# Optimization experiments

Hardware: AMD Instinct MI355X
Metric: run time of the kernel (lower is better)

The kernel has to match this reference:

```python
import jax, jax.numpy as jnp
import numpy as np

B, S, E = 4, 2048, 1024
H, HD, R = 16, 64, 32  # heads, head_dim, rank


def setup_inputs() -> dict:
    key = jax.random.key(0)
    ks = jax.random.split(key, 9)
    sc = 0.02
    return {
        "hidden_states": jax.random.normal(ks[0], (B, S, E), jnp.float32),
        "q_weight": jax.random.normal(ks[1], (E, E), jnp.float32) * sc,
        "q_bias": jax.random.normal(ks[2], (E,), jnp.float32) * sc,
        "k_weight": jax.random.normal(ks[3], (E, E), jnp.float32) * sc,
        "k_bias": jax.random.normal(ks[4], (E,), jnp.float32) * sc,
        "low_rank_value_weight": jax.random.normal(ks[5], (E, H * R), jnp.float32) * sc,
        "low_rank_value_bias": jax.random.normal(ks[6], (H * R,), jnp.float32) * sc,
        "low_rank_output_weight": jax.random.normal(ks[7], (H * R, E), jnp.float32) * sc,
        "output_bias": jax.random.normal(ks[8], (E,), jnp.float32) * sc,
    }


def reference(hidden_states, q_weight, q_bias, k_weight, k_bias,
              low_rank_value_weight, low_rank_value_bias,
              low_rank_output_weight, output_bias):
    b, s, _ = hidden_states.shape
    q = hidden_states @ q_weight + q_bias                       # [B,S,E]
    k = hidden_states @ k_weight + k_bias                       # [B,S,E]
    v = hidden_states @ low_rank_value_weight + low_rank_value_bias  # [B,S,H*R]
    q = q.reshape(b, s, H, HD).transpose(0, 2, 1, 3)            # [B,H,S,HD]
    k = k.reshape(b, s, H, HD).transpose(0, 2, 1, 3)
    v = v.reshape(b, s, H, R).transpose(0, 2, 1, 3)             # [B,H,S,R]
    scores = jnp.einsum('bhqd,bhkd->bhqk', q, k) / jnp.sqrt(jnp.float32(HD))
    causal = jnp.tril(jnp.ones((s, s), dtype=bool))
    scores = jnp.where(causal, scores, jnp.finfo(scores.dtype).min)
    probs = jax.nn.softmax(scores, axis=-1)                     # [B,H,S,S]
    attn = jnp.einsum('bhqk,bhkr->bhqr', probs, v)              # [B,H,S,R]
    attn = attn.transpose(0, 2, 1, 3).reshape(b, s, H * R)      # [B,S,H*R]
    out = attn @ low_rank_output_weight + output_bias           # [B,S,E]
    return out
```

## Files before the change

kernel.cpp:

```cpp
#include <hip/hip_runtime.h>

typedef _Float16 f16;
typedef __attribute__((ext_vector_type(4))) float f4;
typedef __attribute__((ext_vector_type(4))) _Float16 h4;
typedef __attribute__((ext_vector_type(8))) _Float16 h8;
typedef __attribute__((ext_vector_type(4))) float f32x4;
typedef __attribute__((ext_vector_type(4))) unsigned int u4;

extern "C" __device__ __attribute__((const)) float __ocml_native_exp2_f32(float);
#define EXP2F __ocml_native_exp2_f32
#define L2E 1.4426950408889634f

#define SWZ(row, colByte) \
  (((row) << 7) + ((colByte) ^ (((((row) ^ ((row) >> 3))) & 7) << 4)))

__global__ __launch_bounds__(256) void prep(
    const float* __restrict__ hs, f16* __restrict__ hsf,
    const float* __restrict__ qw, const float* __restrict__ kw,
    const float* __restrict__ vw, const float* __restrict__ ow,
    f16* __restrict__ wqkv, f16* __restrict__ owt) {
  const int t = threadIdx.x;
  if (blockIdx.x < 2048) {
    const int n4 = 8192 * 1024 / 4;
    for (int i = blockIdx.x * 256 + t; i < n4; i += 2048 * 256) {
      const f4 v = ((const f4*)hs)[i];
      h4 h;
      h.x = (f16)v.x; h.y = (f16)v.y; h.z = (f16)v.z; h.w = (f16)v.w;
      ((h4*)hsf)[i] = h;
    }
    return;
  }
  __shared__ float tile[32][33];
  int bid = blockIdx.x - 2048;
  const float* in;
  f16* out;
  int R, C, bx, by;
  if (bid < 1024) {
    in = qw; out = wqkv; R = 1024; C = 1024; bx = bid & 31; by = bid >> 5;
  } else if (bid < 2048) {
    bid -= 1024;
    in = kw; out = wqkv + (size_t)1024 * 1024; R = 1024; C = 1024;
    bx = bid & 31; by = bid >> 5;
  } else if (bid < 2560) {
    bid -= 2048;
    in = vw; out = wqkv + (size_t)2048 * 1024; R = 1024; C = 512;
    bx = bid & 15; by = bid >> 4;
  } else {
    bid -= 2560;
    in = ow; out = owt; R = 512; C = 1024; bx = bid & 31; by = bid >> 5;
  }
  const int tx = t & 31, ty = t >> 5;
  const int bc = bx * 32, br = by * 32;
#pragma unroll
  for (int i = 0; i < 4; ++i)
    tile[ty + i * 8][tx] = in[(size_t)(br + ty + i * 8) * C + bc + tx];
  __syncthreads();
#pragma unroll
  for (int i = 0; i < 4; ++i)
    out[(size_t)(bc + ty + i * 8) * R + br + tx] = (f16)tile[tx][ty + i * 8];
}

__global__ __launch_bounds__(256) void hgemm_qkv(
    const f16* __restrict__ A, const f16* __restrict__ Bt,
    const float* __restrict__ qb, const float* __restrict__ kb,
    const float* __restrict__ vb,
    f16* __restrict__ qf, f16* __restrict__ kf, f16* __restrict__ vf) {
  __shared__ f16 As[128 * 40];
  __shared__ f16 Bs[128 * 40];
  const int K = 1024;
  const int id = blockIdx.x;
  const int swz = (id & 7) * 160 + (id >> 3);
  const int bnT = swz % 20;
  const int bm = (swz / 20) * 128;
  const int bn = bnT * 128;
  const int t = threadIdx.x;
  const int lane = t & 63, wave = t >> 6;
  const int wr = wave >> 1, wc = wave & 1;
  const int lrow = lane & 15, lk = lane >> 4;

  f32x4 acc[4][4];
#pragma unroll
  for (int i = 0; i < 4; ++i)
#pragma unroll
    for (int j = 0; j < 4; ++j) acc[i][j] = (f32x4)0.f;

  for (int kt = 0; kt < K; kt += 32) {
#pragma unroll
    for (int i = 0; i < 2; ++i) {
      const int ch = t + i * 256;
      const int row = ch >> 2, part = ch & 3;
      *(u4*)&As[row * 40 + part * 8] =
          *(const u4*)(A + (size_t)(bm + row) * K + kt + part * 8);
      *(u4*)&Bs[row * 40 + part * 8] =
          *(const u4*)(Bt + (size_t)(bn + row) * K + kt + part * 8);
    }
    __syncthreads();
    h8 af[4], bf[4];
#pragma unroll
    for (int f = 0; f < 4; ++f) {
      af[f] = *(const h8*)&As[(wr * 64 + f * 16 + lrow) * 40 + lk * 8];
      bf[f] = *(const h8*)&Bs[(wc * 64 + f * 16 + lrow) * 40 + lk * 8];
    }
#pragma unroll
    for (int i = 0; i < 4; ++i)
#pragma unroll
      for (int j = 0; j < 4; ++j)
        acc[i][j] = __builtin_amdgcn_mfma_f32_16x16x32_f16(af[i], bf[j], acc[i][j], 0, 0, 0);
    __syncthreads();
  }

  const float* bias;
  int nbase;
  if (bnT < 8) { bias = qb; nbase = 0; }
  else if (bnT < 16) { bias = kb; nbase = 1024; }
  else { bias = vb; nbase = 2048; }

#pragma unroll
  for (int fi = 0; fi < 4; ++fi) {
#pragma unroll
    for (int j = 0; j < 4; ++j) {
      const int grow = bm + wr * 64 + fi * 16 + lk * 4 + j;
      const int bb = grow >> 11, ss = grow & 2047;
#pragma unroll
      for (int fj = 0; fj < 4; ++fj) {
        const int gcol = bn + wc * 64 + fj * 16 + lrow;
        const int nl = gcol - nbase;
        const float g = acc[fi][fj][j] + bias[nl];
        if (bnT < 8) {
          qf[((size_t)(bb * 16 + (nl >> 6)) * 2048 + ss) * 64 + (nl & 63)] = (f16)g;
        } else if (bnT < 16) {
          kf[((size_t)(bb * 16 + (nl >> 6)) * 2048 + ss) * 64 + (nl & 63)] = (f16)g;
        } else {
          vf[((size_t)(bb * 16 + (nl >> 5)) * 2048 + ss) * 32 + (nl & 31)] = (f16)g;
        }
      }
    }
  }
}

__global__ __launch_bounds__(256) void transpose_v(
    const f16* __restrict__ vf, f16* __restrict__ vfT) {
  __shared__ f16 tl[32][36];
  const int bh = blockIdx.x >> 6;
  const int st = (blockIdx.x & 63) * 32;
  const int t = threadIdx.x;
  const int row = t >> 3, cq = t & 7;
  {
    const h4 v = *(const h4*)(vf + ((size_t)bh * 2048 + st + row) * 32 + cq * 4);
    *(h4*)&tl[row][cq * 4] = v;
  }
  __syncthreads();
  {
    h4 v;
#pragma unroll
    for (int e = 0; e < 4; ++e) v[e] = tl[cq * 4 + e][row];
    *(h4*)(vfT + ((size_t)bh * 32 + row) * 2048 + st + cq * 4) = v;
  }
}

__global__ __launch_bounds__(256) void hgemm_out(
    const f16* __restrict__ A, const f16* __restrict__ Bt,
    const float* __restrict__ bias, float* __restrict__ outp,
    const int N, const int K) {
  __shared__ f16 As[128 * 40];
  __shared__ f16 Bs[128 * 40];
  const int id = blockIdx.x;
  const int swz = (id & 7) * 64 + (id >> 3);
  const int bn = (swz & 7) * 128;
  const int bm = (swz >> 3) * 128;
  const int t = threadIdx.x;
  const int lane = t & 63, wave = t >> 6;
  const int wr = wave >> 1, wc = wave & 1;
  const int lrow = lane & 15, lk = lane >> 4;

  f32x4 acc[4][4];
#pragma unroll
  for (int i = 0; i < 4; ++i)
#pragma unroll
    for (int j = 0; j < 4; ++j) acc[i][j] = (f32x4)0.f;

  for (int kt = 0; kt < K; kt += 32) {
#pragma unroll
    for (int i = 0; i < 2; ++i) {
      const int ch = t + i * 256;
      const int row = ch >> 2, part = ch & 3;
      *(u4*)&As[row * 40 + part * 8] =
          *(const u4*)(A + (size_t)(bm + row) * K + kt + part * 8);
      *(u4*)&Bs[row * 40 + part * 8] =
          *(const u4*)(Bt + (size_t)(bn + row) * K + kt + part * 8);
    }
    __syncthreads();
    h8 af[4], bf[4];
#pragma unroll
    for (int f = 0; f < 4; ++f) {
      af[f] = *(const h8*)&As[(wr * 64 + f * 16 + lrow) * 40 + lk * 8];
      bf[f] = *(const h8*)&Bs[(wc * 64 + f * 16 + lrow) * 40 + lk * 8];
    }
#pragma unroll
    for (int i = 0; i < 4; ++i)
#pragma unroll
      for (int j = 0; j < 4; ++j)
        acc[i][j] = __builtin_amdgcn_mfma_f32_16x16x32_f16(af[i], bf[j], acc[i][j], 0, 0, 0);
    __syncthreads();
  }

#pragma unroll
  for (int fi = 0; fi < 4; ++fi) {
#pragma unroll
    for (int j = 0; j < 4; ++j) {
      const int grow = bm + wr * 64 + fi * 16 + lk * 4 + j;
#pragma unroll
      for (int fj = 0; fj < 4; ++fj) {
        const int gcol = bn + wc * 64 + fj * 16 + lrow;
        outp[(size_t)grow * N + gcol] = acc[fi][fj][j] + bias[gcol];
      }
    }
  }
}

__global__ __launch_bounds__(256) void attn_mfma(
    const f16* __restrict__ qf, const f16* __restrict__ kf,
    const f16* __restrict__ vfT, f16* __restrict__ attf) {
  __shared__ f16 Ks[64 * 64];
  __shared__ f16 VsT[32 * 64];
  __shared__ f16 Ps[4 * 32 * 64];
  const int id = blockIdx.x;
  const int bh = id & 63;
  const int qblk = 15 - (id >> 6);
  const int qbase = qblk * 128;
  const int t = threadIdx.x;
  const int lane = t & 63, w = t >> 6;
  const int l15 = lane & 15, g = lane >> 4;
  const size_t kvbase = (size_t)bh * 2048;
  char* Pw = (char*)&Ps[w * 32 * 64];

  h8 ones;
#pragma unroll
  for (int e = 0; e < 8; ++e) ones[e] = (f16)1.0f;

  h8 qreg[2][2];
#pragma unroll
  for (int fj = 0; fj < 2; ++fj) {
    const int q = qbase + fj * 64 + w * 16 + l15;
#pragma unroll
    for (int ks = 0; ks < 2; ++ks) {
      h8 raw = *(const h8*)(qf + (kvbase + q) * 64 + ks * 32 + g * 8);
#pragma unroll
      for (int e = 0; e < 8; ++e) raw[e] = raw[e] * (f16)0.125f;
      qreg[fj][ks] = raw;
    }
  }

  f32x4 accO[2][2];
  f32x4 accL[2];
#pragma unroll
  for (int i = 0; i < 2; ++i) {
    accL[i] = (f32x4)0.f;
#pragma unroll
    for (int j = 0; j < 2; ++j) accO[i][j] = (f32x4)0.f;
  }
  float m2[2] = {-1.0e30f, -1.0e30f};

  const int ntiles = qblk * 2 + 2;
  for (int kt = 0; kt < ntiles; ++kt) {
    const int kbase = kt * 64;
    __syncthreads();
#pragma unroll
    for (int i = 0; i < 2; ++i) {
      const int idx = t + i * 256;
      const int row = idx >> 3, ch = idx & 7;
      *(u4*)((char*)Ks + SWZ(row, ch * 16)) =
          *(const u4*)(kf + (kvbase + kbase + row) * 64 + ch * 8);
    }
    {
      const int row = t >> 3, ch = t & 7;
      *(u4*)((char*)VsT + SWZ(row, ch * 16)) =
          *(const u4*)(vfT + ((size_t)bh * 32 + row) * 2048 + kbase + ch * 8);
    }
    __syncthreads();

    f32x4 accS[4][2];
#pragma unroll
    for (int i = 0; i < 4; ++i)
#pragma unroll
      for (int j = 0; j < 2; ++j) accS[i][j] = (f32x4)0.f;
#pragma unroll
    for (int ks = 0; ks < 2; ++ks) {
#pragma unroll
      for (int fim = 0; fim < 4; ++fim) {
        const h8 af = *(const h8*)((char*)Ks + SWZ(fim * 16 + l15, ks * 64 + g * 16));
#pragma unroll
        for (int fj = 0; fj < 2; ++fj)
          accS[fim][fj] = __builtin_amdgcn_mfma_f32_16x16x32_f16(af, qreg[fj][ks], accS[fim][fj], 0, 0, 0);
      }
    }

#pragma unroll
    for (int fj = 0; fj < 2; ++fj) {
      const int qg = qbase + fj * 64 + w * 16 + l15;
      const bool need_mask = (kbase + 63 > qbase + fj * 64 + w * 16);
      float sc[4][4];
#pragma unroll
      for (int fim = 0; fim < 4; ++fim)
#pragma unroll
        for (int j = 0; j < 4; ++j) {
          float v = accS[fim][fj][j];
          if (need_mask) {
            const int key = kbase + fim * 16 + g * 4 + j;
            v = (key <= qg) ? v : -1.0e30f;
          }
          sc[fim][j] = v;
        }
      const float a0 = fmaxf(fmaxf(sc[0][0], sc[0][1]), sc[0][2]);
      const float a1 = fmaxf(fmaxf(sc[0][3], sc[1][0]), sc[1][1]);
      const float a2 = fmaxf(fmaxf(sc[1][2], sc[1][3]), sc[2][0]);
      const float a3 = fmaxf(fmaxf(sc[2][1], sc[2][2]), sc[2][3]);
      const float a4 = fmaxf(fmaxf(sc[3][0], sc[3][1]), sc[3][2]);
      float mc = fmaxf(fmaxf(fmaxf(a0, a1), a2),
                       fmaxf(fmaxf(a3, a4), sc[3][3]));
      mc = fmaxf(mc, __shfl_xor(mc, 16));
      mc = fmaxf(mc, __shfl_xor(mc, 32));
      if (!__all(mc <= m2[fj] + 1.5f)) {
        const float mnew = fmaxf(m2[fj], mc);
        const float corr = __expf(m2[fj] - mnew);
        m2[fj] = mnew;
#pragma unroll
        for (int j = 0; j < 4; ++j) {
          const float c = __shfl(corr, g * 4 + j);
          accO[fj][0][j] *= c;
          accO[fj][1][j] *= c;
          accL[fj][j] *= c;
        }
      }
      const float nml = -m2[fj] * L2E;
#pragma unroll
      for (int fim = 0; fim < 4; ++fim) {
        h4 hp;
#pragma unroll
        for (int j = 0; j < 4; ++j)
          hp[j] = (f16)EXP2F(fmaf(sc[fim][j], L2E, nml));
        *(h4*)(Pw + SWZ(fj * 16 + l15, fim * 32 + g * 8)) = hp;
      }
    }

#pragma unroll
    for (int ks = 0; ks < 2; ++ks) {
      const h8 pa0 = *(const h8*)(Pw + SWZ(l15, ks * 64 + g * 16));
      const h8 pa1 = *(const h8*)(Pw + SWZ(16 + l15, ks * 64 + g * 16));
#pragma unroll
      for (int fr = 0; fr < 2; ++fr) {
        const h8 vb = *(const h8*)((char*)VsT + SWZ(fr * 16 + l15, ks * 64 + g * 16));
        accO[0][fr] = __builtin_amdgcn_mfma_f32_16x16x32_f16(pa0, vb, accO[0][fr], 0, 0, 0);
        accO[1][fr] = __builtin_amdgcn_mfma_f32_16x16x32_f16(pa1, vb, accO[1][fr], 0, 0, 0);
      }
      accL[0] = __builtin_amdgcn_mfma_f32_16x16x32_f16(pa0, ones, accL[0], 0, 0, 0);
      accL[1] = __builtin_amdgcn_mfma_f32_16x16x32_f16(pa1, ones, accL[1], 0, 0, 0);
    }
  }

  const int b = bh >> 4, h = bh & 15;
#pragma unroll
  for (int fo = 0; fo < 2; ++fo) {
#pragma unroll
    for (int j = 0; j < 4; ++j) {
      const float iv = 1.f / accL[fo][j];
      const int q = qbase + fo * 64 + w * 16 + g * 4 + j;
#pragma unroll
      for (int fr = 0; fr < 2; ++fr) {
        const int r = fr * 16 + l15;
        attf[((size_t)b * 2048 + q) * 512 + h * 32 + r] = (f16)(accO[fo][fr][j] * iv);
      }
    }
  }
}

extern "C" void kernel_launch(void* const* d_in, const int* in_sizes, int n_in,
                              void* d_out, int out_size, void* d_ws, size_t ws_size,
                              hipStream_t stream) {
  const float* hs = (const float*)d_in[0];
  const float* qw = (const float*)d_in[1];
  const float* qb = (const float*)d_in[2];
  const float* kw = (const float*)d_in[3];
  const float* kb = (const float*)d_in[4];
  const float* vw = (const float*)d_in[5];
  const float* vb = (const float*)d_in[6];
  const float* ow = (const float*)d_in[7];
  const float* ob = (const float*)d_in[8];
  float* out = (float*)d_out;
  char* ws = (char*)d_ws;

  f16* qf = (f16*)(ws);
  f16* kf = (f16*)(ws + ((size_t)16 << 20));
  f16* vf = (f16*)(ws + ((size_t)32 << 20));
  f16* vfT = (f16*)(ws + ((size_t)72 << 20));
  f16* attf = (f16*)(ws + ((size_t)40 << 20));
  f16* wqkv = (f16*)(ws + ((size_t)48 << 20));
  f16* owt = (f16*)(ws + ((size_t)53 << 20));
  f16* hsf = (f16*)(ws + ((size_t)56 << 20));

  prep<<<dim3(5120), 256, 0, stream>>>(hs, hsf, qw, kw, vw, ow, wqkv, owt);
  hgemm_qkv<<<dim3(1280), 256, 0, stream>>>(hsf, wqkv, qb, kb, vb, qf, kf, vf);
  transpose_v<<<dim3(4096), 256, 0, stream>>>(vf, vfT);
  attn_mfma<<<dim3(1024), 256, 0, stream>>>(qf, kf, vfT, attf);
  hgemm_out<<<dim3(512), 256, 0, stream>>>(attf, owt, ob, out, 1024, 512);
}
```

Baseline: 175.0 us.

## Load QKV GEMM tiles via global_load_lds with pre-swizzled fp16 operands

The prep kernel now writes the fp16 hidden states and the Q/K/V weight rows with an XOR swizzle of 16-byte chunks inside each 64-element group. The QKV GEMM then loads 64-wide K tiles straight from global memory into LDS with global_load_lds, skipping the register round trip. It reads fragments with a matching XOR pattern to avoid bank conflicts. The K step doubles and the LDS tiles grow, but there is still no double buffering, so the loads are still serialized with the MFMA work behind the barriers.

```diff
diff --git a/kernel.cpp b/kernel.cpp
--- a/kernel.cpp
+++ b/kernel.cpp
@@ -13,6 +13,11 @@
 
 #define SWZ(row, colByte) \
   (((row) << 7) + ((colByte) ^ (((((row) ^ ((row) >> 3))) & 7) << 4)))
+
+#define GL16(gp, lp)                                                  \
+  __builtin_amdgcn_global_load_lds(                                   \
+      (const __attribute__((address_space(1))) unsigned int*)(gp),    \
+      (__attribute__((address_space(3))) unsigned int*)(lp), 16, 0, 0)
 
 __global__ __launch_bounds__(256) void prep(
     const float* __restrict__ hs, f16* __restrict__ hsf,
@@ -21,12 +26,18 @@
     f16* __restrict__ wqkv, f16* __restrict__ owt) {
   const int t = threadIdx.x;
   if (blockIdx.x < 2048) {
-    const int n4 = 8192 * 1024 / 4;
-    for (int i = blockIdx.x * 256 + t; i < n4; i += 2048 * 256) {
-      const f4 v = ((const f4*)hs)[i];
-      h4 h;
-      h.x = (f16)v.x; h.y = (f16)v.y; h.z = (f16)v.z; h.w = (f16)v.w;
-      ((h4*)hsf)[i] = h;
+    const int n8 = 8192 * 1024 / 8;
+    for (int c = blockIdx.x * 256 + t; c < n8; c += 2048 * 256) {
+      const int f = c * 8;
+      const int m7 = (f >> 10) & 7;
+      const int cb = (f >> 3) & 7;
+      const f4 v0 = *(const f4*)(hs + f);
+      const f4 v1 = *(const f4*)(hs + f + 4);
+      h8 hv;
+      hv[0] = (f16)v0.x; hv[1] = (f16)v0.y; hv[2] = (f16)v0.z; hv[3] = (f16)v0.w;
+      hv[4] = (f16)v1.x; hv[5] = (f16)v1.y; hv[6] = (f16)v1.z; hv[7] = (f16)v1.w;
+      const int dstf = (f & ~63) | ((cb ^ m7) << 3);
+      *(h8*)(hsf + dstf) = hv;
     }
     return;
   }
@@ -35,6 +46,7 @@
   const float* in;
   f16* out;
   int R, C, bx, by;
+  bool swzout = true;
   if (bid < 1024) {
     in = qw; out = wqkv; R = 1024; C = 1024; bx = bid & 31; by = bid >> 5;
   } else if (bid < 2048) {
@@ -48,6 +60,7 @@
   } else {
     bid -= 2560;
     in = ow; out = owt; R = 512; C = 1024; bx = bid & 31; by = bid >> 5;
+    swzout = false;
   }
   const int tx = t & 31, ty = t >> 5;
   const int bc = bx * 32, br = by * 32;
@@ -56,8 +69,17 @@
     tile[ty + i * 8][tx] = in[(size_t)(br + ty + i * 8) * C + bc + tx];
   __syncthreads();
 #pragma unroll
-  for (int i = 0; i < 4; ++i)
-    out[(size_t)(bc + ty + i * 8) * R + br + tx] = (f16)tile[tx][ty + i * 8];
+  for (int i = 0; i < 4; ++i) {
+    const int n = bc + ty + i * 8;
+    const int k = br + tx;
+    const f16 val = (f16)tile[tx][ty + i * 8];
+    if (swzout) {
+      const int kd = (k & ~63) | (((((k >> 3) & 7) ^ (n & 7))) << 3) | (k & 7);
+      out[(size_t)n * R + kd] = val;
+    } else {
+      out[(size_t)n * R + k] = val;
+    }
+  }
 }
 
 __global__ __launch_bounds__(256) void hgemm_qkv(
@@ -65,8 +87,8 @@
     const float* __restrict__ qb, const float* __restrict__ kb,
     const float* __restrict__ vb,
     f16* __restrict__ qf, f16* __restrict__ kf, f16* __restrict__ vf) {
-  __shared__ f16 As[128 * 40];
-  __shared__ f16 Bs[128 * 40];
+  __shared__ f16 As[128 * 64];
+  __shared__ f16 Bs[128 * 64];
   const int K = 1024;
   const int id = blockIdx.x;
   const int swz = (id & 7) * 160 + (id >> 3);
@@ -77,6 +99,8 @@
   const int lane = t & 63, wave = t >> 6;
   const int wr = wave >> 1, wc = wave & 1;
   const int lrow = lane & 15, lk = lane >> 4;
+  const int srow = lane >> 3;
+  const int scb8 = (lane & 7) * 8;
 
   f32x4 acc[4][4];
 #pragma unroll
@@ -84,29 +108,35 @@
 #pragma unroll
     for (int j = 0; j < 4; ++j) acc[i][j] = (f32x4)0.f;
 
-  for (int kt = 0; kt < K; kt += 32) {
-#pragma unroll
-    for (int i = 0; i < 2; ++i) {
-      const int ch = t + i * 256;
-      const int row = ch >> 2, part = ch & 3;
-      *(u4*)&As[row * 40 + part * 8] =
-          *(const u4*)(A + (size_t)(bm + row) * K + kt + part * 8);
-      *(u4*)&Bs[row * 40 + part * 8] =
-          *(const u4*)(Bt + (size_t)(bn + row) * K + kt + part * 8);
-    }
-    __syncthreads();
-    h8 af[4], bf[4];
-#pragma unroll
-    for (int f = 0; f < 4; ++f) {
-      af[f] = *(const h8*)&As[(wr * 64 + f * 16 + lrow) * 40 + lk * 8];
-      bf[f] = *(const h8*)&Bs[(wc * 64 + f * 16 + lrow) * 40 + lk * 8];
-    }
-#pragma unroll
-    for (int i = 0; i < 4; ++i)
-#pragma unroll
-      for (int j = 0; j < 4; ++j)
-        acc[i][j] = __builtin_amdgcn_mfma_f32_16x16x32_f16(af[i], bf[j], acc[i][j], 0, 0, 0);
-    __syncthreads();
+  for (int kt = 0; kt < K; kt += 64) {
+    __syncthreads();
+#pragma unroll
+    for (int i = 0; i < 4; ++i) {
+      const int r = (wave * 4 + i) * 8 + srow;
+      GL16(A + (size_t)(bm + r) * K + kt + scb8,
+           (char*)As + (wave * 4 + i) * 1024);
+      GL16(Bt + (size_t)(bn + r) * K + kt + scb8,
+           (char*)Bs + (wave * 4 + i) * 1024);
+    }
+    __syncthreads();
+#pragma unroll
+    for (int ks = 0; ks < 2; ++ks) {
+      h8 af[4], bf[4];
+#pragma unroll
+      for (int f = 0; f < 4; ++f) {
+        const int ra = wr * 64 + f * 16 + lrow;
+        af[f] = *(const h8*)((char*)As + ra * 128 +
+                             ((((ks << 2) + lk) ^ (ra & 7)) << 4));
+        const int rb = wc * 64 + f * 16 + lrow;
+        bf[f] = *(const h8*)((char*)Bs + rb * 128 +
+                             ((((ks << 2) + lk) ^ (rb & 7)) << 4));
+      }
+#pragma unroll
+      for (int i2 = 0; i2 < 4; ++i2)
+#pragma unroll
+        for (int j = 0; j < 4; ++j)
+          acc[i2][j] = __builtin_amdgcn_mfma_f32_16x16x32_f16(af[i2], bf[j], acc[i2][j], 0, 0, 0);
+    }
   }
 
   const float* bias;
```

After: 177.2 us. No clear change (+1.3%).

## Double-buffer QKV GEMM with direct global-to-LDS loads and swizzled LDS

Applied to the files above, without the earlier changes.

Replaces the register-staged global→LDS copy in the QKV GEMM with global_load_lds direct transfers into a double-buffered, XOR-swizzled LDS layout. The next K-tile is prefetched while MFMAs run on the current one, synchronised with explicit vmcnt/lgkmcnt waits and barriers. Block-to-tile mapping is also changed to group tiles per XCD for better L2 reuse. The loop issues one extra wasted prefetch on the last iteration (wraps to tile 0), and correctness depends on the hand-tuned waitcnt values.

```diff
diff --git a/kernel.cpp b/kernel.cpp
--- a/kernel.cpp
+++ b/kernel.cpp
@@ -13,6 +13,11 @@
 
 #define SWZ(row, colByte) \
   (((row) << 7) + ((colByte) ^ (((((row) ^ ((row) >> 3))) & 7) << 4)))
+
+#define GL16(gp, lp)                                                  \
+  __builtin_amdgcn_global_load_lds(                                   \
+      (const __attribute__((address_space(1))) unsigned int*)(gp),    \
+      (__attribute__((address_space(3))) unsigned int*)(lp), 16, 0, 0)
 
 __global__ __launch_bounds__(256) void prep(
     const float* __restrict__ hs, f16* __restrict__ hsf,
@@ -65,18 +70,21 @@
     const float* __restrict__ qb, const float* __restrict__ kb,
     const float* __restrict__ vb,
     f16* __restrict__ qf, f16* __restrict__ kf, f16* __restrict__ vf) {
-  __shared__ f16 As[128 * 40];
-  __shared__ f16 Bs[128 * 40];
+  __shared__ f16 As[2 * 128 * 32];
+  __shared__ f16 Bs[2 * 128 * 32];
   const int K = 1024;
   const int id = blockIdx.x;
-  const int swz = (id & 7) * 160 + (id >> 3);
-  const int bnT = swz % 20;
-  const int bm = (swz / 20) * 128;
+  const int xcd = id & 7, loc = id >> 3;
+  const int grp = loc >> 5, inn = loc & 31;
+  const int bnT = grp * 4 + (inn >> 3);
+  const int bm = (xcd * 8 + (inn & 7)) * 128;
   const int bn = bnT * 128;
   const int t = threadIdx.x;
   const int lane = t & 63, wave = t >> 6;
   const int wr = wave >> 1, wc = wave & 1;
   const int lrow = lane & 15, lk = lane >> 4;
+  const int srow = lane >> 2;
+  const int sblk = (lane & 3) ^ ((srow ^ (srow >> 2)) & 3);
 
   f32x4 acc[4][4];
 #pragma unroll
@@ -84,29 +92,42 @@
 #pragma unroll
     for (int j = 0; j < 4; ++j) acc[i][j] = (f32x4)0.f;
 
-  for (int kt = 0; kt < K; kt += 32) {
+  auto stage = [&](int buf, int ktile) {
 #pragma unroll
     for (int i = 0; i < 2; ++i) {
-      const int ch = t + i * 256;
-      const int row = ch >> 2, part = ch & 3;
-      *(u4*)&As[row * 40 + part * 8] =
-          *(const u4*)(A + (size_t)(bm + row) * K + kt + part * 8);
-      *(u4*)&Bs[row * 40 + part * 8] =
-          *(const u4*)(Bt + (size_t)(bn + row) * K + kt + part * 8);
-    }
-    __syncthreads();
+      const int rr = (wave * 2 + i) * 16 + srow;
+      GL16(A + (size_t)(bm + rr) * K + ktile * 32 + sblk * 8,
+           (char*)As + buf * 8192 + (wave * 2 + i) * 1024);
+      GL16(Bt + (size_t)(bn + rr) * K + ktile * 32 + sblk * 8,
+           (char*)Bs + buf * 8192 + (wave * 2 + i) * 1024);
+    }
+  };
+
+  stage(0, 0);
+  for (int kt = 0; kt < 32; ++kt) {
+    const int cur = kt & 1;
+    stage(cur ^ 1, (kt + 1) & 31);
+    asm volatile("s_waitcnt vmcnt(4)" ::: "memory");
+    __builtin_amdgcn_s_barrier();
+    __builtin_amdgcn_sched_barrier(0);
     h8 af[4], bf[4];
 #pragma unroll
     for (int f = 0; f < 4; ++f) {
-      af[f] = *(const h8*)&As[(wr * 64 + f * 16 + lrow) * 40 + lk * 8];
-      bf[f] = *(const h8*)&Bs[(wc * 64 + f * 16 + lrow) * 40 + lk * 8];
-    }
-#pragma unroll
-    for (int i = 0; i < 4; ++i)
+      const int ra = wr * 64 + f * 16 + lrow;
+      af[f] = *(const h8*)((char*)As + cur * 8192 + ra * 64 +
+                           ((lk ^ ((ra ^ (ra >> 2)) & 3)) << 4));
+      const int rb = wc * 64 + f * 16 + lrow;
+      bf[f] = *(const h8*)((char*)Bs + cur * 8192 + rb * 64 +
+                           ((lk ^ ((rb ^ (rb >> 2)) & 3)) << 4));
+    }
+#pragma unroll
+    for (int i2 = 0; i2 < 4; ++i2)
 #pragma unroll
       for (int j = 0; j < 4; ++j)
-        acc[i][j] = __builtin_amdgcn_mfma_f32_16x16x32_f16(af[i], bf[j], acc[i][j], 0, 0, 0);
-    __syncthreads();
+        acc[i2][j] = __builtin_amdgcn_mfma_f32_16x16x32_f16(af[i2], bf[j], acc[i2][j], 0, 0, 0);
+    asm volatile("s_waitcnt lgkmcnt(0)" ::: "memory");
+    __builtin_amdgcn_sched_barrier(0);
+    __builtin_amdgcn_s_barrier();
   }
 
   const float* bias;
```

After: 162.8 us (median of 2 runs). 6.9% less time.
